# Kernel optimization log

Measured on AMD Instinct MI355X. Metric: run time of the kernel, lower is better.

Reference implementation:

```python
import jax, jax.numpy as jnp
import numpy as np

B, N, IN_DIM = 64, 4096, 128
D = 128          # slot_size
S = 7            # num_slots
ITERS = 3
HID = 256        # mlp_hdim
EPS = 1e-8       # renorm epsilon
LN_EPS = 1e-5    # torch LayerNorm default


def _ln(x, g, b):
    m = jnp.mean(x, axis=-1, keepdims=True)
    v = jnp.mean((x - m) ** 2, axis=-1, keepdims=True)
    return (x - m) * jax.lax.rsqrt(v + LN_EPS) * g + b


def setup_inputs() -> dict:
    key = jax.random.key(0)
    ks = jax.random.split(key, 16)
    s = 0.02
    return {
        "x": jax.random.normal(ks[0], (B, N, IN_DIM), jnp.float32),
        "noise": jax.random.normal(ks[1], (B, S, D), jnp.float32),
        "Wq": jax.random.normal(ks[2], (D, D), jnp.float32) * s,
        "Wk": jax.random.normal(ks[3], (D, IN_DIM), jnp.float32) * s,
        "Wv": jax.random.normal(ks[4], (D, IN_DIM), jnp.float32) * s,
        "ln_in_g": jnp.ones((IN_DIM,), jnp.float32),
        "ln_in_b": jnp.zeros((IN_DIM,), jnp.float32),
        "ln_slots_g": jnp.ones((D,), jnp.float32),
        "ln_slots_b": jnp.zeros((D,), jnp.float32),
        "ln_mlp_g": jnp.ones((D,), jnp.float32),
        "ln_mlp_b": jnp.zeros((D,), jnp.float32),
        "W_ih": jax.random.normal(ks[5], (3 * D, D), jnp.float32) * s,
        "W_hh": jax.random.normal(ks[6], (3 * D, D), jnp.float32) * s,
        "b_ih": jnp.zeros((3 * D,), jnp.float32),
        "b_hh": jnp.zeros((3 * D,), jnp.float32),
        "W1": jax.random.normal(ks[7], (HID, D), jnp.float32) * s,
        "b1": jnp.zeros((HID,), jnp.float32),
        "W2": jax.random.normal(ks[8], (D, HID), jnp.float32) * s,
        "b2": jnp.zeros((D,), jnp.float32),
        "mu": jax.random.normal(ks[9], (1, 1, D), jnp.float32) * s,
        "logsigma": jax.random.normal(ks[10], (1, D), jnp.float32) * s,
    }


def reference(x, noise, Wq, Wk, Wv, ln_in_g, ln_in_b, ln_slots_g, ln_slots_b,
              ln_mlp_g, ln_mlp_b, W_ih, W_hh, b_ih, b_hh, W1, b1, W2, b2,
              mu, logsigma):
    xn = _ln(x, ln_in_g, ln_in_b)              # (B,N,IN)
    k = xn @ Wk.T                              # (B,N,D)
    v = xn @ Wv.T                              # (B,N,D)

    scale = jax.nn.softplus(logsigma)[None] + 1e-5   # (1,1,D)
    slots = mu + scale * noise                 # rsample, (B,S,D)

    def gru(u, h):
        gx = u @ W_ih.T + b_ih                 # (B*S, 3D)
        gh = h @ W_hh.T + b_hh
        xr, xz, xn_ = jnp.split(gx, 3, axis=-1)
        hr, hz, hn = jnp.split(gh, 3, axis=-1)
        r = jax.nn.sigmoid(xr + hr)
        z = jax.nn.sigmoid(xz + hz)
        n = jnp.tanh(xn_ + r * hn)
        return (1.0 - z) * n + z * h

    inv_sqrt_d = D ** -0.5
    for _ in range(ITERS):
        slots_prev = slots
        sn = _ln(slots, ln_slots_g, ln_slots_b)
        q = sn @ Wq.T                          # (B,S,D)
        scores = inv_sqrt_d * jnp.einsum('bnd,bsd->bns', k, q)
        attn = jax.nn.softmax(scores, axis=-1)           # over slots
        attn = attn + EPS
        attn = attn / jnp.sum(attn, axis=1, keepdims=True)  # renorm over inputs
        updates = jnp.einsum('bns,bnd->bsd', attn, v)    # (B,S,D)
        h = gru(updates.reshape(-1, D), slots_prev.reshape(-1, D))
        slots = h.reshape(x.shape[0], S, D)
        slots = _ln(slots, ln_mlp_g, ln_mlp_b)
        slots = slots + (jax.nn.relu(slots @ W1.T + b1) @ W2.T + b2)
    return slots
```

## Files before the change

### kernel.cpp

```cpp
#include <hip/hip_runtime.h>
#include <hip/hip_bf16.h>
#include <stdint.h>

#define B_ 64
#define N_ 4096
#define D_ 128
#define S_ 7
#define EPS_ 1e-8f
#define LN_EPS_ 1e-5f
#define SC_INV 0.08838834764831843f

typedef float  f32x4  __attribute__((ext_vector_type(4)));
typedef __bf16 bf16x8 __attribute__((ext_vector_type(8)));

#define WIH_OFF 0
#define WHH_OFF 49152
#define W1_OFF  98304
#define W2_OFF  131072
#define WQ_OFF  163840
#define WKT_OFF 180224
#define WV_OFF  196608
#define WBF_TOT 212992

__device__ __forceinline__ uint16_t f2bfbits(float f) {
    uint32_t x = __float_as_uint(f);
    return (uint16_t)((x + 0x7fffu + ((x >> 16) & 1u)) >> 16);
}
__device__ __forceinline__ uint32_t pk2(float a, float b) {
    return (uint32_t)f2bfbits(a) | ((uint32_t)f2bfbits(b) << 16);
}

__global__ __launch_bounds__(256) void k_init(
    const float* __restrict__ noise, const float* __restrict__ Wk,
    const float* __restrict__ mu, const float* __restrict__ logsigma,
    const float* __restrict__ Wq, const float* __restrict__ lsg,
    const float* __restrict__ lsb,
    const float* __restrict__ Wih, const float* __restrict__ Whh,
    const float* __restrict__ W1, const float* __restrict__ W2,
    const float* __restrict__ Wv,
    float* __restrict__ slots, uint16_t* __restrict__ kqbf,
    uint16_t* __restrict__ wbf) {
    const int t = threadIdx.x;
    const int tid = blockIdx.x * 256 + t;
    const int row = blockIdx.x;
    const int b = row / 7, s = row - b * 7;
    __shared__ float sn[128], qr[128];
    __shared__ float red[2];
    bool act = t < 128;
    float v = 0.f;
    if (act) {
        float sc = log1pf(__expf(logsigma[t])) + 1e-5f;
        v = mu[t] + sc * noise[row * 128 + t];
        slots[row * 128 + t] = v;
    }
    float sv = act ? v : 0.f;
    #pragma unroll
    for (int m = 1; m < 64; m <<= 1) sv += __shfl_xor(sv, m);
    if (act && (t & 63) == 0) red[t >> 6] = sv;
    __syncthreads();
    float mean = (red[0] + red[1]) * (1.0f / 128.0f);
    __syncthreads();
    float dv = act ? (v - mean) : 0.f;
    float sq = dv * dv;
    #pragma unroll
    for (int m = 1; m < 64; m <<= 1) sq += __shfl_xor(sq, m);
    if (act && (t & 63) == 0) red[t >> 6] = sq;
    __syncthreads();
    float var = (red[0] + red[1]) * (1.0f / 128.0f);
    if (act) sn[t] = dv * rsqrtf(var + LN_EPS_) * lsg[t] + lsb[t];
    __syncthreads();
    if (act) {
        const float4* wr = (const float4*)(Wq + t * 128);
        float acc = 0.f;
        #pragma unroll 8
        for (int j = 0; j < 32; ++j) {
            float4 w = wr[j];
            float4 s4 = *(const float4*)(sn + 4 * j);
            acc += w.x * s4.x + w.y * s4.y + w.z * s4.z + w.w * s4.w;
        }
        qr[t] = acc;
    }
    __syncthreads();
    if (act) {
        float kq = 0.f;
        #pragma unroll 8
        for (int o = 0; o < 128; ++o) kq += qr[o] * Wk[o * 128 + t];
        int elem = (t >> 5) * 512 + (s + 16 * ((t >> 3) & 3)) * 8 + (t & 7);
        kqbf[b * 2048 + elem] = f2bfbits(kq * SC_INV);
    }
    if (tid < 73728) {
        int bb = tid / 1152, rem = tid - bb * 1152;
        int sp = 7 + (rem >> 7), d = rem & 127;
        int elem = (d >> 5) * 512 + (sp + 16 * ((d >> 3) & 3)) * 8 + (d & 7);
        kqbf[bb * 2048 + elem] = 0;
    }
    for (int e = tid; e < WBF_TOT; e += 448 * 256) {
        const float* W; int C, el, mode = 0;
        if (e < WHH_OFF)      { W = Wih; C = 128; el = e; }
        else if (e < W1_OFF)  { W = Whh; C = 128; el = e - WHH_OFF; }
        else if (e < W2_OFF)  { W = W1;  C = 128; el = e - W1_OFF; }
        else if (e < WQ_OFF)  { W = W2;  C = 256; el = e - W2_OFF; }
        else if (e < WKT_OFF) { W = Wq;  C = 128; el = e - WQ_OFF; }
        else if (e < WV_OFF)  { W = Wk;  C = 128; el = e - WKT_OFF; mode = 1; }
        else                  { W = Wv;  C = 128; el = e - WV_OFF; }
        int tile = el >> 9, within = el & 511;
        int lp = within >> 3, j = within & 7;
        int lm_ = lp & 15, qd_ = lp >> 4;
        float w;
        if (!mode) {
            int ktN = C >> 5, ot = tile / ktN, kt = tile - ot * ktN;
            w = W[(ot * 16 + lm_) * C + kt * 32 + qd_ * 8 + j];
        } else {
            int dt = tile >> 2, kt = tile & 3;
            w = W[(kt * 32 + qd_ * 8 + j) * 128 + dt * 16 + lm_];
        }
        wbf[e] = f2bfbits(w);
    }
}

__global__ __launch_bounds__(256) void k_prep_xn(
    const float* __restrict__ x, const float* __restrict__ lng,
    const float* __restrict__ lnb, uint16_t* __restrict__ xn) {
    const int t = threadIdx.x, wv = t >> 6, lane = t & 63;
    const int lm = lane & 15, qd = lane >> 4;
    const long row = (long)blockIdx.x * 64 + wv * 16 + lm;
    const long ntile = (long)blockIdx.x * 4 + wv;
    const float* xp = x + row * 128 + qd * 4;
    f32x4 xa[8];
    #pragma unroll
    for (int c = 0; c < 8; ++c) xa[c] = *(const f32x4*)(xp + c * 16);
    float s = 0.f, sq = 0.f;
    #pragma unroll
    for (int c = 0; c < 8; ++c)
        #pragma unroll
        for (int r = 0; r < 4; ++r) { float v = xa[c][r]; s += v; sq += v * v; }
    s  += __shfl_xor(s, 16);  s  += __shfl_xor(s, 32);
    sq += __shfl_xor(sq, 16); sq += __shfl_xor(sq, 32);
    float mean = s * (1.0f / 128.0f);
    float var  = sq * (1.0f / 128.0f) - mean * mean;
    float rs   = rsqrtf(var + LN_EPS_);
    #pragma unroll
    for (int c = 0; c < 8; ++c) {
        f32x4 g  = *(const f32x4*)(lng + c * 16 + qd * 4);
        f32x4 bb = *(const f32x4*)(lnb + c * 16 + qd * 4);
        float v0 = (xa[c][0] - mean) * rs * g[0] + bb[0];
        float v1 = (xa[c][1] - mean) * rs * g[1] + bb[1];
        float v2 = (xa[c][2] - mean) * rs * g[2] + bb[2];
        float v3 = (xa[c][3] - mean) * rs * g[3] + bb[3];
        uint2 st; st.x = pk2(v0, v1); st.y = pk2(v2, v3);
        long elem = (ntile * 4 + (c >> 1)) * 512
                  + (lm + 16 * (2 * (c & 1) + (qd >> 1))) * 8 + 4 * (qd & 1);
        *(uint2*)(xn + elem) = st;
    }
}

__global__ __launch_bounds__(256) void k_attn(
    const uint16_t* __restrict__ xn, const uint16_t* __restrict__ kqbf,
    float* __restrict__ upart, float* __restrict__ cpart) {
    __shared__ __align__(16) uint16_t xns[4][32 * 132];
    __shared__ __align__(16) uint16_t als[4][512];
    __shared__ float part[4][7][132];
    __shared__ float bsum[4][8];
    const int t = threadIdx.x, wv = t >> 6, lane = t & 63;
    const int lm = lane & 15, qd = lane >> 4;
    const int b = blockIdx.x >> 4, chunk = blockIdx.x & 15;
    const int ntb = b * 256 + chunk * 16 + wv * 4;

    bf16x8 kqf[4];
    #pragma unroll
    for (int k0 = 0; k0 < 4; ++k0)
        kqf[k0] = *(const bf16x8*)(kqbf + b * 2048 + k0 * 512 + lane * 8);

    uint16_t* xw = xns[wv];
    f32x4 uacc[8];
    #pragma unroll
    for (int i = 0; i < 8; ++i) uacc[i] = (f32x4){0.f, 0.f, 0.f, 0.f};
    float csl = 0.f;

    #pragma unroll
    for (int sub = 0; sub < 2; ++sub) {
        bf16x8 xf[2][4];
        #pragma unroll
        for (int nt = 0; nt < 2; ++nt)
            #pragma unroll
            for (int k0 = 0; k0 < 4; ++k0)
                xf[nt][k0] = *(const bf16x8*)(xn +
                    ((long)(ntb + sub * 2 + nt) * 4 + k0) * 512 + lane * 8);
        #pragma unroll
        for (int nt = 0; nt < 2; ++nt)
            #pragma unroll
            for (int k0 = 0; k0 < 4; ++k0) {
                int base = (nt * 16 + lm) * 132 + k0 * 32 + qd * 8;
                const uint2* src = (const uint2*)&xf[nt][k0];
                *(uint2*)(xw + base)     = src[0];
                *(uint2*)(xw + base + 4) = src[1];
            }
        #pragma unroll
        for (int mt = 0; mt < 2; ++mt) {
            f32x4 acc = {0.f, 0.f, 0.f, 0.f};
            #pragma unroll
            for (int k0 = 0; k0 < 4; ++k0)
                acc = __builtin_amdgcn_mfma_f32_16x16x32_bf16(xf[mt][k0], kqf[k0], acc, 0, 0, 0);
            uint16_t pb[4];
            #pragma unroll
            for (int r = 0; r < 4; ++r) {
                float sc = acc[r];
                float scm = (lm < 7) ? sc : -1e30f;
                #pragma unroll
                for (int m = 1; m < 16; m <<= 1) scm = fmaxf(scm, __shfl_xor(scm, m));
                float e = (lm < 7) ? __expf(sc - scm) : 0.f;
                float tot = e;
                #pragma unroll
                for (int m = 1; m < 16; m <<= 1) tot += __shfl_xor(tot, m);
                float a_ = e / tot + EPS_;
                if (lm < 7) csl += a_;
                pb[r] = f2bfbits(a_);
            }
            int elem = (lm + 16 * (2 * mt + (qd >> 1))) * 8 + 4 * (qd & 1);
            uint2 pw; pw.x = (uint32_t)pb[0] | ((uint32_t)pb[1] << 16);
            pw.y = (uint32_t)pb[2] | ((uint32_t)pb[3] << 16);
            *(uint2*)(&als[wv][elem]) = pw;
        }
        bf16x8 afr = *(const bf16x8*)(&als[wv][lane * 8]);
        #pragma unroll
        for (int dt = 0; dt < 8; ++dt) {
            bf16x8 bfr;
            #pragma unroll
            for (int j = 0; j < 8; ++j)
                bfr[j] = ((const __bf16*)xw)[(qd * 8 + j) * 132 + dt * 16 + lm];
            uacc[dt] = __builtin_amdgcn_mfma_f32_16x16x32_bf16(afr, bfr, uacc[dt], 0, 0, 0);
        }
    }
    csl += __shfl_xor(csl, 16); csl += __shfl_xor(csl, 32);
    if (lane < 7) bsum[wv][lane] = csl;
    #pragma unroll
    for (int dt = 0; dt < 8; ++dt)
        #pragma unroll
        for (int r = 0; r < 4; ++r) {
            int s = qd * 4 + r;
            if (s < 7) part[wv][s][dt * 16 + lm] = uacc[dt][r];
        }
    __syncthreads();
    if (t < 128) {
        #pragma unroll
        for (int s = 0; s < 7; ++s) {
            float v = part[0][s][t] + part[1][s][t] + part[2][s][t] + part[3][s][t];
            upart[((b * 16 + chunk) * 7 + s) * 128 + t] = v;
        }
    }
    if (t < 7)
        cpart[(b * 16 + chunk) * 7 + t] = bsum[0][t] + bsum[1][t] + bsum[2][t] + bsum[3][t];
}

__global__ __launch_bounds__(256) void k_fused(
    const float* __restrict__ upart, const float* __restrict__ cpart,
    float* __restrict__ slots, const uint16_t* __restrict__ wbf,
    const float* __restrict__ bih, const float* __restrict__ bhh,
    const float* __restrict__ gm, const float* __restrict__ bm,
    const float* __restrict__ b1, const float* __restrict__ b2,
    const float* __restrict__ lsg, const float* __restrict__ lsb,
    uint16_t* __restrict__ kqbf, float* __restrict__ dst, int hasq) {
    __shared__ float uf[16][132];
    __shared__ float hf[16][132];
    __shared__ float slf[16][132];
    __shared__ float hidl[16][264];
    __shared__ float glg[7][776];
    __shared__ float csl[7];
    const int b = blockIdx.x;
    const int t = threadIdx.x, wv = t >> 6, lane = t & 63;
    const int lm = lane & 15, qd = lane >> 4;

    if (t < 7) {
        float c = 0.f;
        #pragma unroll
        for (int i = 0; i < 16; ++i) c += cpart[(b * 16 + i) * 7 + t];
        csl[t] = c;
    }
    for (int idx = t; idx < 896; idx += 256) {
        int s = idx >> 7, d = idx & 127;
        float acc = 0.f;
        #pragma unroll
        for (int i = 0; i < 16; ++i) acc += upart[((b * 16 + i) * 7 + s) * 128 + d];
        slf[s][d] = acc;
        hf[s][d] = slots[(b * 7 + s) * 128 + d];
    }
    __syncthreads();

    {
        bf16x8 apb[4];
        #pragma unroll
        for (int k0 = 0; k0 < 4; ++k0)
            #pragma unroll
            for (int j = 0; j < 8; ++j) apb[k0][j] = (__bf16)slf[lm][k0 * 32 + qd * 8 + j];
        #pragma unroll
        for (int i = 0; i < 2; ++i) {
            int dt = wv * 2 + i;
            f32x4 acc = {0.f, 0.f, 0.f, 0.f};
            #pragma unroll
            for (int k0 = 0; k0 < 4; ++k0) {
                bf16x8 bf = *(const bf16x8*)(wbf + WV_OFF + ((dt * 4 + k0) << 9) + lane * 8);
                acc = __builtin_amdgcn_mfma_f32_16x16x32_bf16(apb[k0], bf, acc, 0, 0, 0);
            }
            #pragma unroll
            for (int r = 0; r < 4; ++r) {
                int s = qd * 4 + r;
                if (s < 7) uf[s][dt * 16 + lm] = acc[r] / csl[s];
            }
        }
    }
    __syncthreads();

    bf16x8 au[4], ah[4];
    #pragma unroll
    for (int k0 = 0; k0 < 4; ++k0)
        #pragma unroll
        for (int j = 0; j < 8; ++j) {
            au[k0][j] = (__bf16)uf[lm][k0 * 32 + qd * 8 + j];
            ah[k0][j] = (__bf16)hf[lm][k0 * 32 + qd * 8 + j];
        }
    {
        const int ih = (wv < 2);
        const uint16_t* W = wbf + (ih ? WIH_OFF : WHH_OFF);
        const int base = ih ? 0 : 384;
        const int w2 = wv & 1;
        #pragma unroll
        for (int i = 0; i < 12; ++i) {
            int ot = w2 * 12 + i;
            f32x4 acc = {0.f, 0.f, 0.f, 0.f};
            #pragma unroll
            for (int k0 = 0; k0 < 4; ++k0) {
                bf16x8 bf = *(const bf16x8*)(W + ((ot * 4 + k0) << 9) + lane * 8);
                acc = __builtin_amdgcn_mfma_f32_16x16x32_bf16(ih ? au[k0] : ah[k0], bf, acc, 0, 0, 0);
            }
            #pragma unroll
            for (int r = 0; r < 4; ++r) {
                int s = qd * 4 + r;
                if (s < 7) glg[s][base + ot * 16 + lm] = acc[r];
            }
        }
    }
    __syncthreads();

    for (int idx = t; idx < 896; idx += 256) {
        int s = idx >> 7, d = idx & 127;
        float xr = glg[s][d] + bih[d];
        float xz = glg[s][128 + d] + bih[128 + d];
        float xg = glg[s][256 + d] + bih[256 + d];
        float hr = glg[s][384 + d] + bhh[d];
        float hz = glg[s][512 + d] + bhh[128 + d];
        float hg = glg[s][640 + d] + bhh[256 + d];
        float r = 1.f / (1.f + __expf(-(xr + hr)));
        float z = 1.f / (1.f + __expf(-(xz + hz)));
        float n = tanhf(xg + r * hg);
        uf[s][d] = (1.f - z) * n + z * hf[s][d];
    }
    __syncthreads();

    for (int s = wv; s < 7; s += 4) {
        float a0 = uf[s][2 * lane], a1 = uf[s][2 * lane + 1];
        float sm = a0 + a1, sq = a0 * a0 + a1 * a1;
        #pragma unroll
        for (int m = 1; m < 64; m <<= 1) { sm += __shfl_xor(sm, m); sq += __shfl_xor(sq, m); }
        float mean = sm * (1.0f / 128.0f);
        float var = sq * (1.0f / 128.0f) - mean * mean;
        float rs = rsqrtf(var + LN_EPS_);
        slf[s][2 * lane]     = (a0 - mean) * rs * gm[2 * lane] + bm[2 * lane];
        slf[s][2 * lane + 1] = (a1 - mean) * rs * gm[2 * lane + 1] + bm[2 * lane + 1];
    }
    __syncthreads();

    bf16x8 as_[4];
    #pragma unroll
    for (int k0 = 0; k0 < 4; ++k0)
        #pragma unroll
        for (int j = 0; j < 8; ++j) as_[k0][j] = (__bf16)slf[lm][k0 * 32 + qd * 8 + j];
    #pragma unroll
    for (int i = 0; i < 4; ++i) {
        int ot = wv * 4 + i;
        f32x4 acc = {0.f, 0.f, 0.f, 0.f};
        #pragma unroll
        for (int k0 = 0; k0 < 4; ++k0) {
            bf16x8 bf = *(const bf16x8*)(wbf + W1_OFF + ((ot * 4 + k0) << 9) + lane * 8);
            acc = __builtin_amdgcn_mfma_f32_16x16x32_bf16(as_[k0], bf, acc, 0, 0, 0);
        }
        #pragma unroll
        for (int r = 0; r < 4; ++r) {
            int s = qd * 4 + r;
            if (s < 7) hidl[s][ot * 16 + lm] = fmaxf(acc[r] + b1[ot * 16 + lm], 0.f);
        }
    }
    __syncthreads();

    bf16x8 ahd[8];
    #pragma unroll
    for (int k0 = 0; k0 < 8; ++k0)
        #pragma unroll
        for (int j = 0; j < 8; ++j) ahd[k0][j] = (__bf16)hidl[lm][k0 * 32 + qd * 8 + j];
    #pragma unroll
    for (int i = 0; i < 2; ++i) {
        int ot = wv * 2 + i;
        f32x4 acc = {0.f, 0.f, 0.f, 0.f};
        #pragma unroll
        for (int k0 = 0; k0 < 8; ++k0) {
            bf16x8 bf = *(const bf16x8*)(wbf + W2_OFF + ((ot * 8 + k0) << 9) + lane * 8);
            acc = __builtin_amdgcn_mfma_f32_16x16x32_bf16(ahd[k0], bf, acc, 0, 0, 0);
        }
        #pragma unroll
        for (int r = 0; r < 4; ++r) {
            int s = qd * 4 + r;
            if (s < 7) {
                float v = slf[s][ot * 16 + lm] + acc[r] + b2[ot * 16 + lm];
                hf[s][ot * 16 + lm] = v;
                dst[(b * 7 + s) * 128 + ot * 16 + lm] = v;
            }
        }
    }
    if (hasq) {
        __syncthreads();
        for (int s = wv; s < 7; s += 4) {
            float a0 = hf[s][2 * lane], a1 = hf[s][2 * lane + 1];
            float sm = a0 + a1, sq = a0 * a0 + a1 * a1;
            #pragma unroll
            for (int m = 1; m < 64; m <<= 1) { sm += __shfl_xor(sm, m); sq += __shfl_xor(sq, m); }
            float mean = sm * (1.0f / 128.0f);
            float var = sq * (1.0f / 128.0f) - mean * mean;
            float rs = rsqrtf(var + LN_EPS_);
            uf[s][2 * lane]     = (a0 - mean) * rs * lsg[2 * lane] + lsb[2 * lane];
            uf[s][2 * lane + 1] = (a1 - mean) * rs * lsg[2 * lane + 1] + lsb[2 * lane + 1];
        }
        __syncthreads();
        bf16x8 an[4];
        #pragma unroll
        for (int k0 = 0; k0 < 4; ++k0)
            #pragma unroll
            for (int j = 0; j < 8; ++j) an[k0][j] = (__bf16)uf[lm][k0 * 32 + qd * 8 + j];
        #pragma unroll
        for (int i = 0; i < 2; ++i) {
            int ot = wv * 2 + i;
            f32x4 acc = {0.f, 0.f, 0.f, 0.f};
            #pragma unroll
            for (int k0 = 0; k0 < 4; ++k0) {
                bf16x8 bf = *(const bf16x8*)(wbf + WQ_OFF + ((ot * 4 + k0) << 9) + lane * 8);
                acc = __builtin_amdgcn_mfma_f32_16x16x32_bf16(an[k0], bf, acc, 0, 0, 0);
            }
            #pragma unroll
            for (int r = 0; r < 4; ++r) {
                int s = qd * 4 + r;
                if (s < 7) slf[s][ot * 16 + lm] = acc[r];
            }
        }
        __syncthreads();
        bf16x8 aq[4];
        #pragma unroll
        for (int k0 = 0; k0 < 4; ++k0)
            #pragma unroll
            for (int j = 0; j < 8; ++j) aq[k0][j] = (__bf16)slf[lm][k0 * 32 + qd * 8 + j];
        #pragma unroll
        for (int i = 0; i < 2; ++i) {
            int dt = wv * 2 + i;
            f32x4 acc = {0.f, 0.f, 0.f, 0.f};
            #pragma unroll
            for (int k0 = 0; k0 < 4; ++k0) {
                bf16x8 bf = *(const bf16x8*)(wbf + WKT_OFF + ((dt * 4 + k0) << 9) + lane * 8);
                acc = __builtin_amdgcn_mfma_f32_16x16x32_bf16(aq[k0], bf, acc, 0, 0, 0);
            }
            #pragma unroll
            for (int r = 0; r < 4; ++r) {
                int s = qd * 4 + r;
                if (s < 7) hidl[s][dt * 16 + lm] = acc[r];
            }
        }
        __syncthreads();
        {
            int kt = t >> 6, lp = t & 63;
            int lmp = lp & 15, qdp = lp >> 4;
            uint16_t h[8];
            #pragma unroll
            for (int j = 0; j < 8; ++j)
                h[j] = (lmp < 7) ? f2bfbits(hidl[lmp][kt * 32 + qdp * 8 + j] * SC_INV) : (uint16_t)0;
            uint4 st;
            st.x = (uint32_t)h[0] | ((uint32_t)h[1] << 16);
            st.y = (uint32_t)h[2] | ((uint32_t)h[3] << 16);
            st.z = (uint32_t)h[4] | ((uint32_t)h[5] << 16);
            st.w = (uint32_t)h[6] | ((uint32_t)h[7] << 16);
            *(uint4*)(kqbf + b * 2048 + t * 8) = st;
        }
    }
}

extern "C" void kernel_launch(void* const* d_in, const int* in_sizes, int n_in,
                              void* d_out, int out_size, void* d_ws, size_t ws_size,
                              hipStream_t stream) {
    const float* x    = (const float*)d_in[0];
    const float* nz   = (const float*)d_in[1];
    const float* Wq   = (const float*)d_in[2];
    const float* Wk   = (const float*)d_in[3];
    const float* Wv   = (const float*)d_in[4];
    const float* ling = (const float*)d_in[5];
    const float* linb = (const float*)d_in[6];
    const float* lsg  = (const float*)d_in[7];
    const float* lsb  = (const float*)d_in[8];
    const float* lmg  = (const float*)d_in[9];
    const float* lmb  = (const float*)d_in[10];
    const float* Wih  = (const float*)d_in[11];
    const float* Whh  = (const float*)d_in[12];
    const float* bih  = (const float*)d_in[13];
    const float* bhh  = (const float*)d_in[14];
    const float* W1   = (const float*)d_in[15];
    const float* b1   = (const float*)d_in[16];
    const float* W2   = (const float*)d_in[17];
    const float* b2   = (const float*)d_in[18];
    const float* mu   = (const float*)d_in[19];
    const float* lsig = (const float*)d_in[20];

    char* wsb = (char*)d_ws;
    uint16_t* xn    = (uint16_t*)(wsb);
    uint16_t* wbf   = (uint16_t*)(wsb + (size_t)67108864);
    uint16_t* kqbf  = (uint16_t*)(wsb + (size_t)67534848);
    float*    slots = (float*)  (wsb + (size_t)67796992);
    float*    upart = (float*)  (wsb + (size_t)68026368);
    float*    cpart = (float*)  (wsb + (size_t)71696384);

    k_init<<<448, 256, 0, stream>>>(nz, Wk, mu, lsig, Wq, lsg, lsb,
                                    Wih, Whh, W1, W2, Wv, slots, kqbf, wbf);
    k_prep_xn<<<4096, 256, 0, stream>>>(x, ling, linb, xn);
    for (int it = 0; it < 3; ++it) {
        float* dst = (it == 2) ? (float*)d_out : slots;
        k_attn<<<1024, 256, 0, stream>>>(xn, kqbf, upart, cpart);
        k_fused<<<64, 256, 0, stream>>>(upart, cpart, slots, wbf, bih, bhh,
                                        lmg, lmb, b1, b2, lsg, lsb,
                                        kqbf, dst, (it < 2) ? 1 : 0);
    }
}
```

Baseline: 374.2 us.

## Precompute transposed xn fragment layout and restructure attention softmax across lanes

```diff
diff --git a/kernel.cpp b/kernel.cpp
--- a/kernel.cpp
+++ b/kernel.cpp
@@ -120,7 +120,9 @@
 
 __global__ __launch_bounds__(256) void k_prep_xn(
     const float* __restrict__ x, const float* __restrict__ lng,
-    const float* __restrict__ lnb, uint16_t* __restrict__ xn) {
+    const float* __restrict__ lnb, uint16_t* __restrict__ xn,
+    uint16_t* __restrict__ xnB) {
+    __shared__ uint16_t sx[64 * 132];
     const int t = threadIdx.x, wv = t >> 6, lane = t & 63;
     const int lm = lane & 15, qd = lane >> 4;
     const long row = (long)blockIdx.x * 64 + wv * 16 + lm;
@@ -151,93 +153,122 @@
         long elem = (ntile * 4 + (c >> 1)) * 512
                   + (lm + 16 * (2 * (c & 1) + (qd >> 1))) * 8 + 4 * (qd & 1);
         *(uint2*)(xn + elem) = st;
-    }
-}
-
-__global__ __launch_bounds__(256) void k_attn(
-    const uint16_t* __restrict__ xn, const uint16_t* __restrict__ kqbf,
+        *(uint2*)(sx + (wv * 16 + lm) * 132 + c * 16 + qd * 4) = st;
+    }
+    __syncthreads();
+    #pragma unroll
+    for (int i = 0; i < 4; ++i) {
+        int tix = i * 4 + wv;
+        int n32l = tix >> 3, dt = tix & 7;
+        uint16_t h[8];
+        #pragma unroll
+        for (int j = 0; j < 8; ++j)
+            h[j] = sx[(n32l * 32 + qd * 8 + j) * 132 + dt * 16 + lm];
+        uint4 stv;
+        stv.x = (uint32_t)h[0] | ((uint32_t)h[1] << 16);
+        stv.y = (uint32_t)h[2] | ((uint32_t)h[3] << 16);
+        stv.z = (uint32_t)h[4] | ((uint32_t)h[5] << 16);
+        stv.w = (uint32_t)h[6] | ((uint32_t)h[7] << 16);
+        *(uint4*)(xnB + ((long)(blockIdx.x * 2 + n32l) * 8 + dt) * 512 + lane * 8) = stv;
+    }
+}
+
+__global__ __launch_bounds__(256, 4) void k_attn(
+    const uint16_t* __restrict__ xn, const uint16_t* __restrict__ xnB,
+    const uint16_t* __restrict__ kqbf,
     float* __restrict__ upart, float* __restrict__ cpart) {
-    __shared__ __align__(16) uint16_t xns[4][32 * 132];
-    __shared__ __align__(16) uint16_t als[4][512];
+    __shared__ __align__(16) uint16_t als[4][16 * 36];
     __shared__ float part[4][7][132];
     __shared__ float bsum[4][8];
     const int t = threadIdx.x, wv = t >> 6, lane = t & 63;
     const int lm = lane & 15, qd = lane >> 4;
     const int b = blockIdx.x >> 4, chunk = blockIdx.x & 15;
     const int ntb = b * 256 + chunk * 16 + wv * 4;
+    const int sbase = qd * 4;
 
     bf16x8 kqf[4];
     #pragma unroll
     for (int k0 = 0; k0 < 4; ++k0)
         kqf[k0] = *(const bf16x8*)(kqbf + b * 2048 + k0 * 512 + lane * 8);
 
-    uint16_t* xw = xns[wv];
+    uint16_t* aw = als[wv];
     f32x4 uacc[8];
     #pragma unroll
     for (int i = 0; i < 8; ++i) uacc[i] = (f32x4){0.f, 0.f, 0.f, 0.f};
-    float csl = 0.f;
+    f32x4 csl = {0.f, 0.f, 0.f, 0.f};
 
     #pragma unroll
     for (int sub = 0; sub < 2; ++sub) {
-        bf16x8 xf[2][4];
-        #pragma unroll
-        for (int nt = 0; nt < 2; ++nt)
+        f32x4 sc[2];
+        #pragma unroll
+        for (int nt = 0; nt < 2; ++nt) {
+            bf16x8 xf[4];
             #pragma unroll
             for (int k0 = 0; k0 < 4; ++k0)
-                xf[nt][k0] = *(const bf16x8*)(xn +
+                xf[k0] = *(const bf16x8*)(xn +
                     ((long)(ntb + sub * 2 + nt) * 4 + k0) * 512 + lane * 8);
-        #pragma unroll
-        for (int nt = 0; nt < 2; ++nt)
-            #pragma unroll
-            for (int k0 = 0; k0 < 4; ++k0) {
-                int base = (nt * 16 + lm) * 132 + k0 * 32 + qd * 8;
-                const uint2* src = (const uint2*)&xf[nt][k0];
-                *(uint2*)(xw + base)     = src[0];
-                *(uint2*)(xw + base + 4) = src[1];
-            }
-        #pragma unroll
-        for (int mt = 0; mt < 2; ++mt) {
             f32x4 acc = {0.f, 0.f, 0.f, 0.f};
             #pragma unroll
             for (int k0 = 0; k0 < 4; ++k0)
-                acc = __builtin_amdgcn_mfma_f32_16x16x32_bf16(xf[mt][k0], kqf[k0], acc, 0, 0, 0);
-            uint16_t pb[4];
+                acc = __builtin_amdgcn_mfma_f32_16x16x32_bf16(kqf[k0], xf[k0], acc, 0, 0, 0);
+            sc[nt] = acc;
+        }
+        const long nb = ((long)(ntb >> 1) + sub) * 8;
+        bf16x8 bb[8];
+        #pragma unroll
+        for (int dt = 0; dt < 8; ++dt)
+            bb[dt] = *(const bf16x8*)(xnB + (nb + dt) * 512 + lane * 8);
+        #pragma unroll
+        for (int nt = 0; nt < 2; ++nt) {
+            float mx = -1e30f;
+            #pragma unroll
+            for (int r = 0; r < 4; ++r)
+                if (sbase + r < 7) mx = fmaxf(mx, sc[nt][r]);
+            mx = fmaxf(mx, __shfl_xor(mx, 16));
+            mx = fmaxf(mx, __shfl_xor(mx, 32));
+            float e[4], tot = 0.f;
             #pragma unroll
             for (int r = 0; r < 4; ++r) {
-                float sc = acc[r];
-                float scm = (lm < 7) ? sc : -1e30f;
-                #pragma unroll
-                for (int m = 1; m < 16; m <<= 1) scm = fmaxf(scm, __shfl_xor(scm, m));
-                float e = (lm < 7) ? __expf(sc - scm) : 0.f;
-                float tot = e;
-                #pragma unroll
-                for (int m = 1; m < 16; m <<= 1) tot += __shfl_xor(tot, m);
-                float a_ = e / tot + EPS_;
-                if (lm < 7) csl += a_;
-                pb[r] = f2bfbits(a_);
-            }
-            int elem = (lm + 16 * (2 * mt + (qd >> 1))) * 8 + 4 * (qd & 1);
-            uint2 pw; pw.x = (uint32_t)pb[0] | ((uint32_t)pb[1] << 16);
-            pw.y = (uint32_t)pb[2] | ((uint32_t)pb[3] << 16);
-            *(uint2*)(&als[wv][elem]) = pw;
-        }
-        bf16x8 afr = *(const bf16x8*)(&als[wv][lane * 8]);
-        #pragma unroll
-        for (int dt = 0; dt < 8; ++dt) {
-            bf16x8 bfr;
-            #pragma unroll
-            for (int j = 0; j < 8; ++j)
-                bfr[j] = ((const __bf16*)xw)[(qd * 8 + j) * 132 + dt * 16 + lm];
-            uacc[dt] = __builtin_amdgcn_mfma_f32_16x16x32_bf16(afr, bfr, uacc[dt], 0, 0, 0);
-        }
-    }
-    csl += __shfl_xor(csl, 16); csl += __shfl_xor(csl, 32);
-    if (lane < 7) bsum[wv][lane] = csl;
+                e[r] = (sbase + r < 7) ? __expf(sc[nt][r] - mx) : 0.f;
+                tot += e[r];
+            }
+            tot += __shfl_xor(tot, 16);
+            tot += __shfl_xor(tot, 32);
+            float inv = 1.0f / tot;
+            #pragma unroll
+            for (int r = 0; r < 4; ++r) {
+                float a_ = (sbase + r < 7) ? e[r] * inv + EPS_ : 0.f;
+                csl[r] += a_;
+                aw[(sbase + r) * 36 + nt * 16 + lm] = f2bfbits(a_);
+            }
+        }
+        union { uint2 u[2]; bf16x8 v; } cva;
+        cva.u[0] = *(const uint2*)(aw + lm * 36 + qd * 8);
+        cva.u[1] = *(const uint2*)(aw + lm * 36 + qd * 8 + 4);
+        bf16x8 afr = cva.v;
+        #pragma unroll
+        for (int dt = 0; dt < 8; ++dt)
+            uacc[dt] = __builtin_amdgcn_mfma_f32_16x16x32_bf16(afr, bb[dt], uacc[dt], 0, 0, 0);
+    }
+    #pragma unroll
+    for (int m = 1; m < 16; m <<= 1) {
+        csl[0] += __shfl_xor(csl[0], m);
+        csl[1] += __shfl_xor(csl[1], m);
+        csl[2] += __shfl_xor(csl[2], m);
+        csl[3] += __shfl_xor(csl[3], m);
+    }
+    if (lm == 0) {
+        #pragma unroll
+        for (int r = 0; r < 4; ++r) {
+            int s = sbase + r;
+            if (s < 7) bsum[wv][s] = csl[r];
+        }
+    }
     #pragma unroll
     for (int dt = 0; dt < 8; ++dt)
         #pragma unroll
         for (int r = 0; r < 4; ++r) {
-            int s = qd * 4 + r;
+            int s = sbase + r;
             if (s < 7) part[wv][s][dt * 16 + lm] = uacc[dt][r];
         }
     __syncthreads();
@@ -515,18 +546,19 @@
 
     char* wsb = (char*)d_ws;
     uint16_t* xn    = (uint16_t*)(wsb);
-    uint16_t* wbf   = (uint16_t*)(wsb + (size_t)67108864);
-    uint16_t* kqbf  = (uint16_t*)(wsb + (size_t)67534848);
-    float*    slots = (float*)  (wsb + (size_t)67796992);
-    float*    upart = (float*)  (wsb + (size_t)68026368);
-    float*    cpart = (float*)  (wsb + (size_t)71696384);
+    uint16_t* xnB   = (uint16_t*)(wsb + (size_t)67108864);
+    uint16_t* wbf   = (uint16_t*)(wsb + (size_t)134217728);
+    uint16_t* kqbf  = (uint16_t*)(wsb + (size_t)134643712);
+    float*    slots = (float*)  (wsb + (size_t)134905856);
+    float*    upart = (float*)  (wsb + (size_t)135135232);
+    float*    cpart = (float*)  (wsb + (size_t)138805248);
 
     k_init<<<448, 256, 0, stream>>>(nz, Wk, mu, lsig, Wq, lsg, lsb,
                                     Wih, Whh, W1, W2, Wv, slots, kqbf, wbf);
-    k_prep_xn<<<4096, 256, 0, stream>>>(x, ling, linb, xn);
+    k_prep_xn<<<4096, 256, 0, stream>>>(x, ling, linb, xn, xnB);
     for (int it = 0; it < 3; ++it) {
         float* dst = (it == 2) ? (float*)d_out : slots;
-        k_attn<<<1024, 256, 0, stream>>>(xn, kqbf, upart, cpart);
+        k_attn<<<1024, 256, 0, stream>>>(xn, xnB, kqbf, upart, cpart);
         k_fused<<<64, 256, 0, stream>>>(upart, cpart, slots, wbf, bih, bhh,
                                         lmg, lmb, b1, b2, lsg, lsb,
                                         kqbf, dst, (it < 2) ? 1 : 0);
```

After: 410.5 us. +9.7%, slower.
